# Kernel tuning notes

Measured on AMD Instinct MI355X. Metric: run time of the kernel, lower is better.

## Reference

```python
import jax, jax.numpy as jnp
import numpy as np
from jax import lax

NUM_EXPERT = 2   # top-k experts kept per image
N_EXPERTS = 4    # total experts


def setup_inputs() -> dict:
    key = jax.random.key(0)
    ks = jax.random.split(key, 4)
    B, C, H, W = 16, 64, 128, 128
    inputs = jax.random.normal(ks[0], (B, C, H, W), dtype=jnp.float32)
    k = jax.random.uniform(ks[1], (B, C, 1, 1), dtype=jnp.float32)
    gate_w = jax.random.normal(ks[2], (N_EXPERTS, C), dtype=jnp.float32) * (1.0 / np.sqrt(C))
    gate_b = jnp.zeros((N_EXPERTS,), dtype=jnp.float32)
    conv_w = jax.random.normal(ks[3], (N_EXPERTS, C, C, 3, 3), dtype=jnp.float32) * (1.0 / np.sqrt(C * 9))
    conv_b = jnp.zeros((N_EXPERTS, C), dtype=jnp.float32)
    return {"inputs": inputs, "k": k, "gate_w": gate_w, "gate_b": gate_b,
            "conv_w": conv_w, "conv_b": conv_b}


def _expert(x, k, w, b):
    # expert_i(x, k) = ReLU(Conv3x3_i(x) + b_i) * k   (FiLM-style conditioning)
    y = lax.conv_general_dilated(x, w, window_strides=(1, 1), padding='SAME',
                                 dimension_numbers=('NCHW', 'OIHW', 'NCHW'))
    return jax.nn.relu(y + b[None, :, None, None]) * k


def reference(inputs, k, gate_w, gate_b, conv_w, conv_b):
    B = inputs.shape[0]
    # gate: global average pool over HW, then linear C -> E
    pooled = inputs.mean(axis=(2, 3))                       # [B, C]
    logits = pooled @ gate_w.T + gate_b                     # [B, E]
    # softmax in float32 (matches F.softmax(..., dtype=torch.float))
    weights = jax.nn.softmax(logits.astype(jnp.float32), axis=1).astype(inputs.dtype)
    topk_w, topk_idx = lax.top_k(weights, NUM_EXPERT)       # [B, num_expert]
    # scatter top-k weights into a dense [B, E] mask (zeros elsewhere)
    exp_weights = jnp.zeros_like(weights).at[jnp.arange(B)[:, None], topk_idx].set(topk_w)
    # dense loop over ALL experts, weighted sum with mostly-zero weights
    out = inputs
    for i in range(N_EXPERTS):
        out = out + _expert(inputs, k, conv_w[i], conv_b[i]) * exp_weights[:, i, None, None, None]
    return out
```

## Files before the change

### kernel.cpp

```cpp
#include <hip/hip_runtime.h>

typedef __attribute__((ext_vector_type(8))) short bfrag8;
typedef __attribute__((ext_vector_type(4))) short bfrag4;
typedef __attribute__((ext_vector_type(16))) float f32x16;

#define B_ 16
#define C_ 64
#define H_ 128
#define W_ 128
#define E_ 4
#define HW_ (H_ * W_)

#define NSL 66
#define PLANE2 (NSL * 16)
#define ROWB2  (8 * PLANE2)
#define RG 4

#define WT_ELEMS (4 * 9 * 2 * 4 * 64 * 8)
#define OFF_POOL (WT_ELEMS * 2)
#define OFF_EW   (OFF_POOL + 1024 * 4)
#define WS_NEEDED ((size_t)(OFF_EW + 64 * 4))

#define FB_WT_OFF 0
#define FB_POOLED_OFF 147456
#define FB_EW_OFF 148480

__device__ inline unsigned short f2bf(float f) {
    unsigned u = __builtin_bit_cast(unsigned, f);
    unsigned r = u + 0x7FFFu + ((u >> 16) & 1u);
    return (unsigned short)(r >> 16);
}
__device__ inline float bf2f(unsigned short s) {
    return __builtin_bit_cast(float, (unsigned)s << 16);
}

__global__ __launch_bounds__(256) void pool_wcvt(const float* __restrict__ in,
                                                 const float* __restrict__ cw,
                                                 float* __restrict__ pooled,
                                                 unsigned short* __restrict__ wT2) {
    if (blockIdx.x < 576) {
        const int idx = blockIdx.x * 256 + threadIdx.x;
        const int j = idx & 7;
        const int l = (idx >> 3) & 63;
        const int f = idx >> 9;
        const int kb = f & 3;
        const int chh = (f >> 2) & 1;
        const int et = f >> 3;
        const int tap = et % 9;
        const int e = et / 9;
        const int co = chh * 32 + (l & 31);
        const int ci = kb * 16 + (l >> 5) * 8 + j;
        wT2[idx] = f2bf(cw[(((e * C_ + co) * C_ + ci) * 9) + tap]);
    }
    const int bc = blockIdx.x;
    const float* p = in + (size_t)bc * HW_;
    float s = 0.f;
    for (int i = threadIdx.x; i < HW_ / 4; i += 256) {
        float4 v = ((const float4*)p)[i];
        s += v.x + v.y + v.z + v.w;
    }
    for (int off = 32; off; off >>= 1) s += __shfl_down(s, off);
    __shared__ float red[4];
    const int lane = threadIdx.x & 63, wv = threadIdx.x >> 6;
    if (lane == 0) red[wv] = s;
    __syncthreads();
    if (threadIdx.x == 0)
        pooled[bc] = (red[0] + red[1] + red[2] + red[3]) * (1.0f / (float)HW_);
}

__global__ void gate_kernel(const float* __restrict__ pooled,
                            const float* __restrict__ gate_w,
                            const float* __restrict__ gate_b,
                            float* __restrict__ ew) {
    const int b = threadIdx.x;
    if (b >= B_) return;
    float lg[E_];
    for (int e = 0; e < E_; e++) {
        float s = gate_b[e];
        for (int c = 0; c < C_; c++) s += pooled[b * C_ + c] * gate_w[e * C_ + c];
        lg[e] = s;
    }
    float m = fmaxf(fmaxf(lg[0], lg[1]), fmaxf(lg[2], lg[3]));
    float ex[E_], sum = 0.f;
    for (int e = 0; e < E_; e++) { ex[e] = expf(lg[e] - m); sum += ex[e]; }
    for (int e = 0; e < E_; e++) ex[e] /= sum;
    int i1 = 0;
    for (int e = 1; e < E_; e++) if (ex[e] > ex[i1]) i1 = e;
    int i2 = -1;
    for (int e = 0; e < E_; e++) {
        if (e == i1) continue;
        if (i2 < 0 || ex[e] > ex[i2]) i2 = e;
    }
    for (int e = 0; e < E_; e++)
        ew[b * E_ + e] = (e == i1 || e == i2) ? ex[e] : 0.f;
}

__global__ __launch_bounds__(256, 2) void conv_p4(const float* __restrict__ in,
                                                  const float* __restrict__ kk,
                                                  const float* __restrict__ cb,
                                                  const float* __restrict__ pooled,
                                                  const float* __restrict__ gw,
                                                  const float* __restrict__ gb,
                                                  const unsigned short* __restrict__ wT2,
                                                  float* __restrict__ out) {
    const int raw = blockIdx.x;
    const int swz = (raw & 7) * 128 + (raw >> 3);
    const int b   = swz >> 6;
    const int pxh = (swz >> 5) & 1;
    const int h0  = (swz & 31) * RG;
    const int x0g = pxh * 64;

    const int tid = threadIdx.x;
    const int lane = tid & 63;
    const int wv = tid >> 6;
    const int ln = lane & 31;
    const int lh = lane >> 5;
    const int ch = wv & 1;
    const int pq = wv >> 1;
    const int co0 = ch * 32;

    const int spx = tid & 63;
    const int scg = tid >> 6;

    __shared__ __align__(16) char ring[4 * ROWB2];
    __shared__ float sEW[E_];

    if (tid < 64) {
        const float p = pooled[b * C_ + lane];
        float part[E_];
#pragma unroll
        for (int e = 0; e < E_; e++) part[e] = p * gw[e * C_ + lane];
#pragma unroll
        for (int off = 32; off; off >>= 1)
#pragma unroll
            for (int e = 0; e < E_; e++) part[e] += __shfl_down(part[e], off);
        if (lane == 0) {
            float lg[E_];
#pragma unroll
            for (int e = 0; e < E_; e++) lg[e] = part[e] + gb[e];
            float m = fmaxf(fmaxf(lg[0], lg[1]), fmaxf(lg[2], lg[3]));
            float ex[E_], sum = 0.f;
#pragma unroll
            for (int e = 0; e < E_; e++) { ex[e] = __expf(lg[e] - m); sum += ex[e]; }
            const float inv = 1.0f / sum;
            int i1 = 0;
            for (int e = 1; e < E_; e++) if (ex[e] > ex[i1]) i1 = e;
            int i2 = -1;
            for (int e = 0; e < E_; e++) {
                if (e == i1) continue;
                if (i2 < 0 || ex[e] > ex[i2]) i2 = e;
            }
#pragma unroll
            for (int e = 0; e < E_; e++)
                sEW[e] = (e == i1 || e == i2) ? ex[e] * inv : 0.f;
        }
    }
    __syncthreads();

    int e0 = 0, e1 = 0; float w0 = 0.f, w1 = 0.f;
    {
        int found = 0;
        for (int e = 0; e < E_; e++) {
            float we = sEW[e];
            if (we != 0.f) {
                if (!found) { e0 = e; w0 = we; found = 1; }
                else        { e1 = e; w1 = we; }
            }
        }
        if (w1 == 0.f) e1 = e0;
    }

    const float* cb0 = cb + e0 * C_;
    const float* cb1 = cb + e1 * C_;
    const float* kkp = kk + b * C_;

    float pv[16], ph[8];
    auto STAGE = [&](int r) {
        if ((unsigned)r < (unsigned)H_) {
            const float* src = in + ((size_t)(b * C_ + scg * 16) * H_ + r) * W_ + x0g + spx;
#pragma unroll
            for (int i = 0; i < 16; ++i) pv[i] = src[(size_t)i * HW_];
        } else {
#pragma unroll
            for (int i = 0; i < 16; ++i) pv[i] = 0.f;
        }
        if (tid < 16) {
            const int hp = tid & 1;
            const int cgh = tid >> 1;
            const int pg = hp ? (x0g + 64) : (x0g - 1);
            const bool ok = ((unsigned)r < (unsigned)H_) && ((unsigned)pg < (unsigned)W_);
            const float* src = in + ((size_t)(b * C_ + cgh * 8) * H_ + (((unsigned)r < (unsigned)H_) ? r : 0)) * W_ + (ok ? pg : 0);
#pragma unroll
            for (int i = 0; i < 8; ++i) ph[i] = ok ? src[(size_t)i * HW_] : 0.f;
        }
    };
    auto COMMIT = [&](int rs) {
        bfrag8 f0, f1;
#pragma unroll
        for (int j = 0; j < 8; ++j) {
            f0[j] = (short)f2bf(pv[j]);
            f1[j] = (short)f2bf(pv[8 + j]);
        }
        char* bp = ring + rs * ROWB2 + (spx + 1) * 16;
        *(bfrag8*)(bp + (scg * 2) * PLANE2) = f0;
        *(bfrag8*)(bp + (scg * 2 + 1) * PLANE2) = f1;
        if (tid < 16) {
            const int hp = tid & 1, cgh = tid >> 1;
            bfrag8 g;
#pragma unroll
            for (int i = 0; i < 8; ++i) g[i] = (short)f2bf(ph[i]);
            *(bfrag8*)(ring + rs * ROWB2 + cgh * PLANE2 + (hp ? 65 : 0) * 16) = g;
        }
    };

    STAGE(h0 - 1); COMMIT(0);
    STAGE(h0);     COMMIT(1);
    STAGE(h0 + 1); COMMIT(2);
    __syncthreads();

    const char* wb0 = (const char*)wT2 + (size_t)e0 * 73728 + ch * 4096 + lane * 16;
    const char* wb1 = (const char*)wT2 + (size_t)e1 * 73728 + ch * 4096 + lane * 16;

    for (int s = 0; s < RG; ++s) {
        if (s + 1 < RG) STAGE(h0 + s + 2);

        f32x16 Ae0, Ae1;
#pragma unroll
        for (int i = 0; i < 16; ++i) { Ae0[i] = 0.f; Ae1[i] = 0.f; }

#pragma unroll 1
        for (int ky = 0; ky < 3; ++ky) {
            const char* rb = ring + ((s + ky) & 3) * ROWB2;
            const char* wk0 = wb0 + ky * 24576;
            const char* wk1 = wb1 + ky * 24576;
#pragma unroll 1
            for (int kx = 0; kx < 3; ++kx) {
#pragma unroll
                for (int kb = 0; kb < 4; ++kb) {
                    bfrag8 a0 = *(const bfrag8*)(wk0 + kx * 8192 + kb * 1024);
                    bfrag8 a1 = *(const bfrag8*)(wk1 + kx * 8192 + kb * 1024);
                    bfrag8 bb = *(const bfrag8*)(rb + (kb * 2 + lh) * PLANE2
                                                 + (pq * 32 + ln + kx) * 16);
                    Ae0 = __builtin_amdgcn_mfma_f32_32x32x16_bf16(a0, bb, Ae0, 0, 0, 0);
                    Ae1 = __builtin_amdgcn_mfma_f32_32x32x16_bf16(a1, bb, Ae1, 0, 0, 0);
                }
            }
        }

        if (s + 1 < RG) COMMIT((s + 3) & 3);

        const int row = h0 + s;
        const char* rm1 = ring + ((s + 1) & 3) * ROWB2 + (pq * 32 + ln + 1) * 16 + lh * 8;
        bfrag4 ra[4];
#pragma unroll
        for (int c = 0; c < 4; ++c)
            ra[c] = *(const bfrag4*)(rm1 + (ch * 4 + c) * PLANE2);
#pragma unroll
        for (int g = 0; g < 16; ++g) {
            const int r_ = g & 3, c_ = g >> 2;
            const int co = co0 + r_ + 8 * c_ + 4 * lh;
            const float kv = kkp[co];
            const size_t oi = ((size_t)(b * C_ + co) * H_ + row) * W_ + x0g + pq * 32 + ln;
            out[oi] = bf2f((unsigned short)ra[c_][r_])
                      + fmaxf(Ae0[g] + cb0[co], 0.f) * (kv * w0)
                      + fmaxf(Ae1[g] + cb1[co], 0.f) * (kv * w1);
        }

        __syncthreads();
    }
}

#define CHUNK 32

__global__ __launch_bounds__(256) void pool_kernel(const float* __restrict__ in,
                                                   float* __restrict__ pooled) {
    const int bc = blockIdx.x;
    const float* p = in + (size_t)bc * HW_;
    float s = 0.f;
    for (int i = threadIdx.x; i < HW_ / 4; i += 256) {
        float4 v = ((const float4*)p)[i];
        s += v.x + v.y + v.z + v.w;
    }
    for (int off = 32; off; off >>= 1) s += __shfl_down(s, off);
    __shared__ float red[4];
    const int lane = threadIdx.x & 63, wv = threadIdx.x >> 6;
    if (lane == 0) red[wv] = s;
    __syncthreads();
    if (threadIdx.x == 0)
        pooled[bc] = (red[0] + red[1] + red[2] + red[3]) * (1.0f / (float)HW_);
}

__global__ __launch_bounds__(256) void wtr_kernel(const float* __restrict__ cw,
                                                  float* __restrict__ wT) {
    const int idx = blockIdx.x * 256 + threadIdx.x;
    if (idx >= E_ * C_ * 9 * C_) return;
    const int co = idx & 63;
    const int t2 = idx >> 6;
    const int tap = t2 % 9;
    const int t3 = t2 / 9;
    const int ci = t3 & 63;
    const int e = t3 >> 6;
    wT[idx] = cw[(((e * C_ + co) * C_ + ci) * 9) + tap];
}

__global__ __launch_bounds__(512) void conv_fallback(const float* __restrict__ in,
                                                     const float* __restrict__ kk,
                                                     const float* __restrict__ wT,
                                                     const float* __restrict__ cb,
                                                     const float* __restrict__ ew,
                                                     float* __restrict__ out) {
    const int bid = blockIdx.x;
    const int b = bid / H_;
    const int h = bid % H_;
    const int tid = threadIdx.x;
    const int lane = tid & 63;
    const int wv = tid >> 6;
    const int x0 = wv * 16;

    __shared__ float sIn[CHUNK * 3 * W_];

    float w0 = 0.f, w1 = 0.f;
    int e0 = 0, e1 = 0;
    {
        float we[E_];
#pragma unroll
        for (int e = 0; e < E_; e++) we[e] = ew[b * E_ + e];
        int found = 0;
        for (int e = 0; e < E_; e++) {
            if (we[e] != 0.f) {
                if (!found) { e0 = e; w0 = we[e]; found = 1; }
                else        { e1 = e; w1 = we[e]; }
            }
        }
        if (w1 == 0.f) e1 = e0;
    }

    float acc0[16], acc1[16];
#pragma unroll
    for (int i = 0; i < 16; i++) { acc0[i] = 0.f; acc1[i] = 0.f; }

    for (int cblk = 0; cblk < C_ / CHUNK; cblk++) {
        const int cbase = cblk * CHUNK;
        __syncthreads();
        for (int f = tid; f < CHUNK * 3 * W_ / 4; f += 512) {
            const int fi = f * 4;
            const int ci = fi / (3 * W_);
            const int rem = fi - ci * 3 * W_;
            const int kyy = rem / W_;
            const int x = rem - kyy * W_;
            const int hh = h + kyy - 1;
            float4 v = make_float4(0.f, 0.f, 0.f, 0.f);
            if (hh >= 0 && hh < H_)
                v = *(const float4*)(in + ((size_t)(b * C_ + cbase + ci) * H_ + hh) * W_ + x);
            *(float4*)(sIn + fi) = v;
        }
        __syncthreads();

        const float* wp0 = wT + (size_t)((e0 * C_ + cbase) * 9) * C_ + lane;
        const float* wp1 = wT + (size_t)((e1 * C_ + cbase) * 9) * C_ + lane;
        for (int ci = 0; ci < CHUNK; ci++) {
            float wa[9], wb[9];
#pragma unroll
            for (int t = 0; t < 9; t++) {
                wa[t] = wp0[(ci * 9 + t) * C_];
                wb[t] = wp1[(ci * 9 + t) * C_];
            }
            const float* rowp = sIn + ci * 3 * W_;
#pragma unroll
            for (int kyy = 0; kyy < 3; kyy++) {
                float xin[18];
                const float* rp = rowp + kyy * W_ + x0;
                xin[0] = (x0 == 0) ? 0.f : rp[-1];
#pragma unroll
                for (int j = 0; j < 16; j += 4) {
                    float4 v = *(const float4*)(rp + j);
                    xin[1 + j] = v.x; xin[2 + j] = v.y; xin[3 + j] = v.z; xin[4 + j] = v.w;
                }
                xin[17] = (x0 + 16 >= W_) ? 0.f : rp[16];
                const int t0 = kyy * 3;
#pragma unroll
                for (int x = 0; x < 16; x++) {
                    acc0[x] += xin[x] * wa[t0] + xin[x + 1] * wa[t0 + 1] + xin[x + 2] * wa[t0 + 2];
                    acc1[x] += xin[x] * wb[t0] + xin[x + 1] * wb[t0 + 1] + xin[x + 2] * wb[t0 + 2];
                }
            }
        }
    }

    const float kv = kk[b * C_ + lane];
    const float b0v = cb[e0 * C_ + lane];
    const float b1v = cb[e1 * C_ + lane];
    const float kw0 = kv * w0, kw1 = kv * w1;
    const size_t obase = ((size_t)(b * C_ + lane) * H_ + h) * W_ + x0;
#pragma unroll
    for (int x = 0; x < 16; x += 4) {
        float4 iv = *(const float4*)(in + obase + x);
        float4 ov;
        ov.x = iv.x + fmaxf(acc0[x + 0] + b0v, 0.f) * kw0 + fmaxf(acc1[x + 0] + b1v, 0.f) * kw1;
        ov.y = iv.y + fmaxf(acc0[x + 1] + b0v, 0.f) * kw0 + fmaxf(acc1[x + 1] + b1v, 0.f) * kw1;
        ov.z = iv.z + fmaxf(acc0[x + 2] + b0v, 0.f) * kw0 + fmaxf(acc1[x + 2] + b1v, 0.f) * kw1;
        ov.w = iv.w + fmaxf(acc0[x + 3] + b0v, 0.f) * kw0 + fmaxf(acc1[x + 3] + b1v, 0.f) * kw1;
        *(float4*)(out + obase + x) = ov;
    }
}

extern "C" void kernel_launch(void* const* d_in, const int* in_sizes, int n_in,
                              void* d_out, int out_size, void* d_ws, size_t ws_size,
                              hipStream_t stream) {
    const float* inputs = (const float*)d_in[0];
    const float* k      = (const float*)d_in[1];
    const float* gate_w = (const float*)d_in[2];
    const float* gate_b = (const float*)d_in[3];
    const float* conv_w = (const float*)d_in[4];
    const float* conv_b = (const float*)d_in[5];
    float* out = (float*)d_out;
    char* wsb = (char*)d_ws;

    if (ws_size >= WS_NEEDED) {
        unsigned short* wT2 = (unsigned short*)wsb;
        float* pooled = (float*)(wsb + OFF_POOL);

        pool_wcvt<<<B_ * C_, 256, 0, stream>>>(inputs, conv_w, pooled, wT2);
        conv_p4<<<1024, 256, 0, stream>>>(inputs, k, conv_b, pooled,
                                          gate_w, gate_b, wT2, out);
    } else {
        float* ws = (float*)d_ws;
        float* wTf    = ws + FB_WT_OFF;
        float* pooled = ws + FB_POOLED_OFF;
        float* ewbuf  = ws + FB_EW_OFF;

        pool_kernel<<<B_ * C_, 256, 0, stream>>>(inputs, pooled);
        gate_kernel<<<1, 64, 0, stream>>>(pooled, gate_w, gate_b, ewbuf);
        wtr_kernel<<<(E_ * C_ * 9 * C_ + 255) / 256, 256, 0, stream>>>(conv_w, wTf);
        conv_fallback<<<B_ * H_, 512, 0, stream>>>(inputs, k, wTf, conv_b, ewbuf, out);
    }
}
```

Before: 82.65 us.

## Process two output rows per block with 512 threads and six-row ring

Doubles the block to 512 threads, with two groups of four waves each computing a different output row concurrently. Each block now covers 8 rows instead of 4, so the halo rows staged into shared memory are amortised over more output. Staging loads two input rows per step into a six-slot ring. This cuts the grid to 512 blocks, which reduces redundant halo loads and barrier counts but raises LDS use per block and may lower the number of resident blocks.

```diff
diff --git a/kernel.cpp b/kernel.cpp
--- a/kernel.cpp
+++ b/kernel.cpp
@@ -14,7 +14,8 @@
 #define NSL 66
 #define PLANE2 (NSL * 16)
 #define ROWB2  (8 * PLANE2)
-#define RG 4
+#define RG 8
+#define NRS 6
 
 #define WT_ELEMS (4 * 9 * 2 * 4 * 64 * 8)
 #define OFF_POOL (WT_ELEMS * 2)
@@ -95,7 +96,7 @@
         ew[b * E_ + e] = (e == i1 || e == i2) ? ex[e] : 0.f;
 }
 
-__global__ __launch_bounds__(256, 2) void conv_p4(const float* __restrict__ in,
+__global__ __launch_bounds__(512, 2) void conv_2r(const float* __restrict__ in,
                                                   const float* __restrict__ kk,
                                                   const float* __restrict__ cb,
                                                   const float* __restrict__ pooled,
@@ -104,10 +105,10 @@
                                                   const unsigned short* __restrict__ wT2,
                                                   float* __restrict__ out) {
     const int raw = blockIdx.x;
-    const int swz = (raw & 7) * 128 + (raw >> 3);
-    const int b   = swz >> 6;
-    const int pxh = (swz >> 5) & 1;
-    const int h0  = (swz & 31) * RG;
+    const int swz = (raw & 7) * 64 + (raw >> 3);
+    const int b   = swz >> 5;
+    const int pxh = (swz >> 4) & 1;
+    const int h0  = (swz & 15) * RG;
     const int x0g = pxh * 64;
 
     const int tid = threadIdx.x;
@@ -115,14 +116,16 @@
     const int wv = tid >> 6;
     const int ln = lane & 31;
     const int lh = lane >> 5;
-    const int ch = wv & 1;
-    const int pq = wv >> 1;
+    const int rh = wv >> 2;
+    const int ch = (wv >> 1) & 1;
+    const int pq = wv & 1;
     const int co0 = ch * 32;
 
     const int spx = tid & 63;
-    const int scg = tid >> 6;
-
-    __shared__ __align__(16) char ring[4 * ROWB2];
+    const int scg = (tid >> 6) & 3;
+    const int srow = tid >> 8;
+
+    __shared__ __align__(16) char ring[NRS * ROWB2];
     __shared__ float sEW[E_];
 
     if (tid < 64) {
@@ -175,7 +178,8 @@
     const float* kkp = kk + b * C_;
 
     float pv[16], ph[8];
-    auto STAGE = [&](int r) {
+    auto STAGE = [&](int pr) {
+        const int r = pr + srow;
         if ((unsigned)r < (unsigned)H_) {
             const float* src = in + ((size_t)(b * C_ + scg * 16) * H_ + r) * W_ + x0g + spx;
 #pragma unroll
@@ -184,45 +188,52 @@
 #pragma unroll
             for (int i = 0; i < 16; ++i) pv[i] = 0.f;
         }
-        if (tid < 16) {
+        if (tid < 32) {
             const int hp = tid & 1;
-            const int cgh = tid >> 1;
+            const int cgh = (tid >> 1) & 7;
+            const int hrow = tid >> 4;
+            const int rr = pr + hrow;
             const int pg = hp ? (x0g + 64) : (x0g - 1);
-            const bool ok = ((unsigned)r < (unsigned)H_) && ((unsigned)pg < (unsigned)W_);
-            const float* src = in + ((size_t)(b * C_ + cgh * 8) * H_ + (((unsigned)r < (unsigned)H_) ? r : 0)) * W_ + (ok ? pg : 0);
+            const bool ok = ((unsigned)rr < (unsigned)H_) && ((unsigned)pg < (unsigned)W_);
+            const float* src = in + ((size_t)(b * C_ + cgh * 8) * H_ + (((unsigned)rr < (unsigned)H_) ? rr : 0)) * W_ + (ok ? pg : 0);
 #pragma unroll
             for (int i = 0; i < 8; ++i) ph[i] = ok ? src[(size_t)i * HW_] : 0.f;
         }
     };
-    auto COMMIT = [&](int rs) {
+    auto COMMIT = [&](int sl0) {
+        int sl = sl0 + srow; if (sl >= NRS) sl -= NRS;
         bfrag8 f0, f1;
 #pragma unroll
         for (int j = 0; j < 8; ++j) {
             f0[j] = (short)f2bf(pv[j]);
             f1[j] = (short)f2bf(pv[8 + j]);
         }
-        char* bp = ring + rs * ROWB2 + (spx + 1) * 16;
+        char* bp = ring + sl * ROWB2 + (spx + 1) * 16;
         *(bfrag8*)(bp + (scg * 2) * PLANE2) = f0;
         *(bfrag8*)(bp + (scg * 2 + 1) * PLANE2) = f1;
-        if (tid < 16) {
-            const int hp = tid & 1, cgh = tid >> 1;
+        if (tid < 32) {
+            const int hp = tid & 1;
+            const int cgh = (tid >> 1) & 7;
+            const int hrow = tid >> 4;
+            int slh = sl0 + hrow; if (slh >= NRS) slh -= NRS;
             bfrag8 g;
 #pragma unroll
             for (int i = 0; i < 8; ++i) g[i] = (short)f2bf(ph[i]);
-            *(bfrag8*)(ring + rs * ROWB2 + cgh * PLANE2 + (hp ? 65 : 0) * 16) = g;
+            *(bfrag8*)(ring + slh * ROWB2 + cgh * PLANE2 + (hp ? 65 : 0) * 16) = g;
         }
     };
 
     STAGE(h0 - 1); COMMIT(0);
-    STAGE(h0);     COMMIT(1);
     STAGE(h0 + 1); COMMIT(2);
     __syncthreads();
 
     const char* wb0 = (const char*)wT2 + (size_t)e0 * 73728 + ch * 4096 + lane * 16;
     const char* wb1 = (const char*)wT2 + (size_t)e1 * 73728 + ch * 4096 + lane * 16;
 
-    for (int s = 0; s < RG; ++s) {
-        if (s + 1 < RG) STAGE(h0 + s + 2);
+    for (int t = 0; t < RG / 2; ++t) {
+        if (t + 1 < RG / 2) STAGE(h0 + 2 * t + 3);
+
+        const int myloc = 2 * t + rh;
 
         f32x16 Ae0, Ae1;
 #pragma unroll
@@ -230,7 +241,8 @@
 
 #pragma unroll 1
         for (int ky = 0; ky < 3; ++ky) {
-            const char* rb = ring + ((s + ky) & 3) * ROWB2;
+            int u = myloc + ky; if (u >= NRS) u -= NRS;
+            const char* rb = ring + u * ROWB2;
             const char* wk0 = wb0 + ky * 24576;
             const char* wk1 = wb1 + ky * 24576;
 #pragma unroll 1
@@ -247,10 +259,14 @@
             }
         }
 
-        if (s + 1 < RG) COMMIT((s + 3) & 3);
-
-        const int row = h0 + s;
-        const char* rm1 = ring + ((s + 1) & 3) * ROWB2 + (pq * 32 + ln + 1) * 16 + lh * 8;
+        if (t + 1 < RG / 2) {
+            int sl0 = 2 * t + 4; if (sl0 >= NRS) sl0 -= NRS;
+            COMMIT(sl0);
+        }
+
+        const int row = h0 + 2 * t + rh;
+        int v = myloc + 1; if (v >= NRS) v -= NRS;
+        const char* rm1 = ring + v * ROWB2 + (pq * 32 + ln + 1) * 16 + lh * 8;
         bfrag4 ra[4];
 #pragma unroll
         for (int c = 0; c < 4; ++c)
@@ -421,8 +437,8 @@
         float* pooled = (float*)(wsb + OFF_POOL);
 
         pool_wcvt<<<B_ * C_, 256, 0, stream>>>(inputs, conv_w, pooled, wT2);
-        conv_p4<<<1024, 256, 0, stream>>>(inputs, k, conv_b, pooled,
-                                          gate_w, gate_b, wT2, out);
+        conv_2r<<<512, 512, 0, stream>>>(inputs, k, conv_b, pooled,
+                                         gate_w, gate_b, wT2, out);
     } else {
         float* ws = (float*)d_ws;
         float* wTf    = ws + FB_WT_OFF;
```

New measurement: 84.14 us. Within noise of the previous version (+1.8%).

## Double-buffer row staging with five-slot LDS ring and unrolled pipeline

Applied to the files above, without the earlier changes.

Reworks the conv kernel's row pipeline so two register staging buffers alternate, keeping global loads for future rows in flight across more than one MFMA step. The LDS ring grows from four to five row slots and the row loop is fully unrolled into an explicit schedule. __syncthreads is replaced by a custom barrier that waits only on LDS counters. Launch bounds drop to one block per SIMD-set hint, which trades occupancy for more registers. The risk is fewer resident waves to hide latency and higher register and LDS use per block.

```diff
diff --git a/kernel.cpp b/kernel.cpp
--- a/kernel.cpp
+++ b/kernel.cpp
@@ -15,6 +15,12 @@
 #define PLANE2 (NSL * 16)
 #define ROWB2  (8 * PLANE2)
 #define RG 4
+#define NRS 5
+
+#define BARRIER() do { \
+    asm volatile("s_waitcnt lgkmcnt(0)" ::: "memory"); \
+    __builtin_amdgcn_s_barrier(); \
+} while (0)
 
 #define WT_ELEMS (4 * 9 * 2 * 4 * 64 * 8)
 #define OFF_POOL (WT_ELEMS * 2)
@@ -95,14 +101,14 @@
         ew[b * E_ + e] = (e == i1 || e == i2) ? ex[e] : 0.f;
 }
 
-__global__ __launch_bounds__(256, 2) void conv_p4(const float* __restrict__ in,
-                                                  const float* __restrict__ kk,
-                                                  const float* __restrict__ cb,
-                                                  const float* __restrict__ pooled,
-                                                  const float* __restrict__ gw,
-                                                  const float* __restrict__ gb,
-                                                  const unsigned short* __restrict__ wT2,
-                                                  float* __restrict__ out) {
+__global__ __launch_bounds__(256, 1) void conv_pipe(const float* __restrict__ in,
+                                                    const float* __restrict__ kk,
+                                                    const float* __restrict__ cb,
+                                                    const float* __restrict__ pooled,
+                                                    const float* __restrict__ gw,
+                                                    const float* __restrict__ gb,
+                                                    const unsigned short* __restrict__ wT2,
+                                                    float* __restrict__ out) {
     const int raw = blockIdx.x;
     const int swz = (raw & 7) * 128 + (raw >> 3);
     const int b   = swz >> 6;
@@ -122,7 +128,7 @@
     const int spx = tid & 63;
     const int scg = tid >> 6;
 
-    __shared__ __align__(16) char ring[4 * ROWB2];
+    __shared__ __align__(16) char ring[NRS * ROWB2];
     __shared__ float sEW[E_];
 
     if (tid < 64) {
@@ -174,32 +180,50 @@
     const float* cb1 = cb + e1 * C_;
     const float* kkp = kk + b * C_;
 
-    float pv[16], ph[8];
-    auto STAGE = [&](int r) {
+    float pvA[16], phA[8], pvB[16], phB[8];
+
+    auto STAGEA = [&](int r) {
         if ((unsigned)r < (unsigned)H_) {
             const float* src = in + ((size_t)(b * C_ + scg * 16) * H_ + r) * W_ + x0g + spx;
 #pragma unroll
-            for (int i = 0; i < 16; ++i) pv[i] = src[(size_t)i * HW_];
+            for (int i = 0; i < 16; ++i) pvA[i] = src[(size_t)i * HW_];
         } else {
 #pragma unroll
-            for (int i = 0; i < 16; ++i) pv[i] = 0.f;
+            for (int i = 0; i < 16; ++i) pvA[i] = 0.f;
         }
         if (tid < 16) {
-            const int hp = tid & 1;
-            const int cgh = tid >> 1;
+            const int hp = tid & 1, cgh = tid >> 1;
             const int pg = hp ? (x0g + 64) : (x0g - 1);
             const bool ok = ((unsigned)r < (unsigned)H_) && ((unsigned)pg < (unsigned)W_);
             const float* src = in + ((size_t)(b * C_ + cgh * 8) * H_ + (((unsigned)r < (unsigned)H_) ? r : 0)) * W_ + (ok ? pg : 0);
 #pragma unroll
-            for (int i = 0; i < 8; ++i) ph[i] = ok ? src[(size_t)i * HW_] : 0.f;
+            for (int i = 0; i < 8; ++i) phA[i] = ok ? src[(size_t)i * HW_] : 0.f;
         }
     };
-    auto COMMIT = [&](int rs) {
+    auto STAGEB = [&](int r) {
+        if ((unsigned)r < (unsigned)H_) {
+            const float* src = in + ((size_t)(b * C_ + scg * 16) * H_ + r) * W_ + x0g + spx;
+#pragma unroll
+            for (int i = 0; i < 16; ++i) pvB[i] = src[(size_t)i * HW_];
+        } else {
+#pragma unroll
+            for (int i = 0; i < 16; ++i) pvB[i] = 0.f;
+        }
+        if (tid < 16) {
+            const int hp = tid & 1, cgh = tid >> 1;
+            const int pg = hp ? (x0g + 64) : (x0g - 1);
+            const bool ok = ((unsigned)r < (unsigned)H_) && ((unsigned)pg < (unsigned)W_);
+            const float* src = in + ((size_t)(b * C_ + cgh * 8) * H_ + (((unsigned)r < (unsigned)H_) ? r : 0)) * W_ + (ok ? pg : 0);
+#pragma unroll
+            for (int i = 0; i < 8; ++i) phB[i] = ok ? src[(size_t)i * HW_] : 0.f;
+        }
+    };
+    auto COMMITA = [&](int rs) {
         bfrag8 f0, f1;
 #pragma unroll
         for (int j = 0; j < 8; ++j) {
-            f0[j] = (short)f2bf(pv[j]);
-            f1[j] = (short)f2bf(pv[8 + j]);
+            f0[j] = (short)f2bf(pvA[j]);
+            f1[j] = (short)f2bf(pvA[8 + j]);
         }
         char* bp = ring + rs * ROWB2 + (spx + 1) * 16;
         *(bfrag8*)(bp + (scg * 2) * PLANE2) = f0;
@@ -208,29 +232,40 @@
             const int hp = tid & 1, cgh = tid >> 1;
             bfrag8 g;
 #pragma unroll
-            for (int i = 0; i < 8; ++i) g[i] = (short)f2bf(ph[i]);
+            for (int i = 0; i < 8; ++i) g[i] = (short)f2bf(phA[i]);
             *(bfrag8*)(ring + rs * ROWB2 + cgh * PLANE2 + (hp ? 65 : 0) * 16) = g;
         }
     };
-
-    STAGE(h0 - 1); COMMIT(0);
-    STAGE(h0);     COMMIT(1);
-    STAGE(h0 + 1); COMMIT(2);
-    __syncthreads();
+    auto COMMITB = [&](int rs) {
+        bfrag8 f0, f1;
+#pragma unroll
+        for (int j = 0; j < 8; ++j) {
+            f0[j] = (short)f2bf(pvB[j]);
+            f1[j] = (short)f2bf(pvB[8 + j]);
+        }
+        char* bp = ring + rs * ROWB2 + (spx + 1) * 16;
+        *(bfrag8*)(bp + (scg * 2) * PLANE2) = f0;
+        *(bfrag8*)(bp + (scg * 2 + 1) * PLANE2) = f1;
+        if (tid < 16) {
+            const int hp = tid & 1, cgh = tid >> 1;
+            bfrag8 g;
+#pragma unroll
+            for (int i = 0; i < 8; ++i) g[i] = (short)f2bf(phB[i]);
+            *(bfrag8*)(ring + rs * ROWB2 + cgh * PLANE2 + (hp ? 65 : 0) * 16) = g;
+        }
+    };
 
     const char* wb0 = (const char*)wT2 + (size_t)e0 * 73728 + ch * 4096 + lane * 16;
     const char* wb1 = (const char*)wT2 + (size_t)e1 * 73728 + ch * 4096 + lane * 16;
 
-    for (int s = 0; s < RG; ++s) {
-        if (s + 1 < RG) STAGE(h0 + s + 2);
-
+    auto DO_STEP = [&](int s0, int row) {
         f32x16 Ae0, Ae1;
 #pragma unroll
         for (int i = 0; i < 16; ++i) { Ae0[i] = 0.f; Ae1[i] = 0.f; }
-
 #pragma unroll 1
         for (int ky = 0; ky < 3; ++ky) {
-            const char* rb = ring + ((s + ky) & 3) * ROWB2;
+            int u = s0 + ky; if (u >= NRS) u -= NRS;
+            const char* rb = ring + u * ROWB2;
             const char* wk0 = wb0 + ky * 24576;
             const char* wk1 = wb1 + ky * 24576;
 #pragma unroll 1
@@ -246,11 +281,8 @@
                 }
             }
         }
-
-        if (s + 1 < RG) COMMIT((s + 3) & 3);
-
-        const int row = h0 + s;
-        const char* rm1 = ring + ((s + 1) & 3) * ROWB2 + (pq * 32 + ln + 1) * 16 + lh * 8;
+        int v = s0 + 1; if (v >= NRS) v -= NRS;
+        const char* rm1 = ring + v * ROWB2 + (pq * 32 + ln + 1) * 16 + lh * 8;
         bfrag4 ra[4];
 #pragma unroll
         for (int c = 0; c < 4; ++c)
@@ -265,9 +297,29 @@
                       + fmaxf(Ae0[g] + cb0[co], 0.f) * (kv * w0)
                       + fmaxf(Ae1[g] + cb1[co], 0.f) * (kv * w1);
         }
-
-        __syncthreads();
-    }
+    };
+
+    STAGEA(h0 - 1);
+    STAGEB(h0);
+    COMMITA(0);
+    STAGEA(h0 + 1);
+    COMMITB(1);
+    STAGEB(h0 + 2);
+    COMMITA(2);
+    BARRIER();
+
+    STAGEA(h0 + 3);
+    COMMITB(3);
+    DO_STEP(0, h0 + 0);
+    BARRIER();
+    STAGEB(h0 + 4);
+    COMMITA(4);
+    DO_STEP(1, h0 + 1);
+    BARRIER();
+    COMMITB(0);
+    DO_STEP(2, h0 + 2);
+    BARRIER();
+    DO_STEP(3, h0 + 3);
 }
 
 #define CHUNK 32
@@ -421,8 +473,8 @@
         float* pooled = (float*)(wsb + OFF_POOL);
 
         pool_wcvt<<<B_ * C_, 256, 0, stream>>>(inputs, conv_w, pooled, wT2);
-        conv_p4<<<1024, 256, 0, stream>>>(inputs, k, conv_b, pooled,
-                                          gate_w, gate_b, wT2, out);
+        conv_pipe<<<1024, 256, 0, stream>>>(inputs, k, conv_b, pooled,
+                                            gate_w, gate_b, wT2, out);
     } else {
         float* ws = (float*)d_ws;
         float* wTf    = ws + FB_WT_OFF;
```

Result: slower. 87.17 us (+5.5%).
